# Kernel optimization log

Hardware: AMD Instinct MI355X
Metric: run time of the kernel (lower is better)

Reference implementation:

```python
import jax, jax.numpy as jnp
import numpy as np

B, V, E = 8, 12288, 147456
C_FM, C_U, C_IN, C_HID, C_OUT = 384, 61, 64, 128, 32
EPS = 0.005


def grid_sample_bilinear(img, grid):
    """torch.F.grid_sample, mode='bilinear', padding='zeros', align_corners=False.
    img: (B,C,H,W); grid: (B,Hg,Wg,2) in [-1,1] (x,y). Returns (B,C,Hg,Wg)."""
    Bn, C, H, W = img.shape
    x = (grid[..., 0] + 1.0) * 0.5 * W - 0.5
    y = (grid[..., 1] + 1.0) * 0.5 * H - 0.5
    x0 = jnp.floor(x); y0 = jnp.floor(y)
    wx1 = x - x0; wy1 = y - y0
    wx0 = 1.0 - wx1; wy0 = 1.0 - wy1
    x0i = x0.astype(jnp.int32); y0i = y0.astype(jnp.int32)

    def gather(iy, ix):
        valid = (ix >= 0) & (ix < W) & (iy >= 0) & (iy < H)
        ixc = jnp.clip(ix, 0, W - 1)
        iyc = jnp.clip(iy, 0, H - 1)
        v = jax.vmap(lambda im, yy, xx: im[:, yy, xx])(img, iyc, ixc)  # (B,C,Hg,Wg)
        return v * valid[:, None].astype(img.dtype)

    out = (gather(y0i, x0i) * (wy0 * wx0)[:, None]
           + gather(y0i, x0i + 1) * (wy0 * wx1)[:, None]
           + gather(y0i + 1, x0i) * (wy1 * wx0)[:, None]
           + gather(y0i + 1, x0i + 1) * (wy1 * wx1)[:, None])
    return out


def setup_inputs() -> dict:
    key = jax.random.key(0)
    ks = jax.random.split(key, 12)
    vertices = jax.random.normal(ks[0], (B, V, 3), jnp.float32) * 0.3
    fz = jnp.full((B,), 0.005, jnp.float32) + jax.random.uniform(ks[1], (B,), jnp.float32) * 0.0005
    cz = jax.random.normal(ks[2], (B, 2), jnp.float32) * 0.05
    # depth near fz*(z+100) ~ 0.5 so the |d - z| < eps visibility test fires for a subset
    depth_map = 0.5 + jax.random.normal(ks[3], (B, 1, 128, 128), jnp.float32) * 0.005
    feature_map = jax.random.normal(ks[4], (B, C_FM, 64, 64), jnp.float32)
    conv_w = jax.random.normal(ks[5], (C_U, C_FM), jnp.float32) / np.sqrt(C_FM)
    conv_b = jnp.zeros((C_U,), jnp.float32)
    W1 = jax.random.normal(ks[6], (C_IN, C_HID), jnp.float32) / np.sqrt(C_IN)
    b1 = jnp.zeros((C_HID,), jnp.float32)
    W2 = jax.random.normal(ks[7], (C_HID, C_OUT), jnp.float32) / np.sqrt(C_HID)
    W_dv = jax.random.normal(ks[8], (C_HID, 3), jnp.float32) / np.sqrt(C_HID)
    edge_row = jax.random.randint(ks[9], (E,), 0, V, jnp.int32)
    edge_col = jax.random.randint(ks[10], (E,), 0, V, jnp.int32)
    return {"feature_map": feature_map, "depth_map": depth_map, "vertices": vertices,
            "fz": fz, "cz": cz, "conv_w": conv_w, "conv_b": conv_b,
            "W1": W1, "b1": b1, "W2": W2, "W_dv": W_dv,
            "edge_row": edge_row, "edge_col": edge_col}


def reference(feature_map, depth_map, vertices, fz, cz, conv_w, conv_b,
              W1, b1, W2, W_dv, edge_row, edge_col):
    # ---- indexing(): project vertices to image plane (replicates cz[:,0] on both axes as in source) ----
    v = jnp.stack([vertices[..., 0], vertices[..., 1], vertices[..., 2] + 100.0], axis=-1)
    v = fz[:, None, None] * v
    cshift = cz[:, 0][:, None]
    v = v.at[..., 0].add(cshift).at[..., 1].add(cshift)
    grid = v[:, None, :, :2]                                     # (B,1,V,2)
    sampled_depth = grid_sample_bilinear(depth_map, grid)[:, 0, 0, :]   # (B,V)
    visible = jnp.abs(sampled_depth - v[..., 2]) < EPS           # (B,V) bool
    sf = grid_sample_bilinear(feature_map, grid)[:, :, 0, :]     # (B,C_FM,V)
    sf = sf * visible[:, None, :].astype(sf.dtype)
    # ---- 1x1 conv projection ----
    proj = jnp.einsum('oc,bcv->bov', conv_w, sf) + conv_b[None, :, None]  # (B,C_U,V)
    # ---- GCN input: concat projected features + raw vertex coords ----
    x = jnp.concatenate([proj, jnp.transpose(vertices, (0, 2, 1))], axis=1)  # (B,C_IN,V)
    x = jnp.transpose(x, (0, 2, 1))                              # (B,V,C_IN)
    # ---- sparse-adjacency message passing (row-normalized A) ----
    deg = jax.ops.segment_sum(jnp.ones((E,), x.dtype), edge_row, num_segments=V)
    deg = jnp.maximum(deg, 1.0)

    def agg(h):  # h: (B,V,C) -> A_norm @ h
        msgs = h[:, edge_col]                                    # (B,E,C) gather
        s = jax.vmap(lambda m: jax.ops.segment_sum(m, edge_row, num_segments=V))(msgs)
        return s / deg[None, :, None]

    h = jax.nn.relu(agg(x) @ W1 + b1)                            # (B,V,C_HID)
    x_out = agg(h) @ W2                                          # (B,V,C_OUT)
    dv = h @ W_dv                                                # (B,V,3)
    vertices_new = vertices + dv
    # pack (gcn features, refined verts *1000, offsets *1000) as in source scaling
    return jnp.concatenate([x_out, vertices_new * 1000.0, dv * 1000.0], axis=-1)  # (B,V,38)
```

## Files before the change

kernel.cpp:

```cpp
#include <hip/hip_runtime.h>

#define NB 8
#define NV 12288
#define NE 147456
#define CFM 384
#define CU 61
#define FEPS 0.005f

typedef unsigned short ushort_t;
typedef unsigned int uint_t;
typedef __attribute__((ext_vector_type(8))) unsigned short ushort8v;
typedef __attribute__((ext_vector_type(4))) unsigned short ushort4v;

__device__ inline float b2f(ushort_t u) {
    return __uint_as_float(((uint_t)u) << 16);
}
__device__ inline ushort_t f2b(float f) {
    uint_t u = __float_as_uint(f);
    return (ushort_t)((u + 0x7fffu + ((u >> 16) & 1u)) >> 16);
}

__global__ __launch_bounds__(512) void kL1(const float* __restrict__ cw,
                                           float* __restrict__ cwT,
                                           const int* __restrict__ erow,
                                           int* __restrict__ counts) {
    if (blockIdx.x < 48) {
        int idx = blockIdx.x * 512 + threadIdx.x;
        int c = idx >> 6, o = idx & 63;
        cwT[idx] = (o < CU) ? cw[o * CFM + c] : 0.f;
    } else {
        int e = (blockIdx.x - 48) * 512 + threadIdx.x;
        if (e < NE) atomicAdd(&counts[erow[e]], 1);
    }
}

__device__ void conv_body(int bid, float* smem, const float* __restrict__ fm,
                          const float* __restrict__ cwT, ushort_t* __restrict__ pf) {
    int tid = threadIdx.x;
    int lane = tid & 63;
    int og = __builtin_amdgcn_readfirstlane(tid >> 6);
    int idx0 = bid * 64;
    int b = idx0 >> 12, p0 = idx0 & 4095;
    const float* fb = fm + (size_t)b * CFM * 4096 + p0;
    int sc = tid >> 4, spq = tid & 15;
    const float* saddr = fb + (size_t)sc * 4096 + spq * 4;

    float acc[8];
#pragma unroll
    for (int o = 0; o < 8; o++) acc[o] = 0.f;

    float4 nxt = *(const float4*)saddr;
    int buf = 0;
    for (int cc = 0; cc < CFM; cc += 32) {
        float* ftb = smem + buf * 2048;
        *(float4*)(ftb + sc * 64 + spq * 4) = nxt;
        __syncthreads();
        if (cc + 32 < CFM)
            nxt = *(const float4*)(saddr + (size_t)(cc + 32) * 4096);
#pragma unroll 8
        for (int c = 0; c < 32; c++) {
            float fv = ftb[c * 64 + lane];
            const float4* w4 = (const float4*)(cwT + (cc + c) * 64 + og * 8);
            float4 wa = w4[0], wb = w4[1];
            float w[8] = {wa.x, wa.y, wa.z, wa.w, wb.x, wb.y, wb.z, wb.w};
#pragma unroll
            for (int o = 0; o < 8; o++) acc[o] = fmaf(fv, w[o], acc[o]);
        }
        buf ^= 1;
    }
    uint_t pk[4];
#pragma unroll
    for (int j = 0; j < 4; j++)
        pk[j] = (uint_t)f2b(acc[2 * j]) | ((uint_t)f2b(acc[2 * j + 1]) << 16);
    uint4* outp = (uint4*)(pf + (size_t)(idx0 + lane) * 64 + og * 8);
    outp[0] = make_uint4(pk[0], pk[1], pk[2], pk[3]);
}

__device__ void scan_body(int* ipart, const int* __restrict__ counts,
                          int* __restrict__ offs) {
    int t = threadIdx.x;
    int base = t * 24;
    int local[24];
    int s = 0;
#pragma unroll
    for (int i = 0; i < 24; i++) { local[i] = s; s += counts[base + i]; }
    ipart[t] = s;
    __syncthreads();
    for (int off = 1; off < 512; off <<= 1) {
        int v = (t >= off) ? ipart[t - off] : 0;
        __syncthreads();
        ipart[t] += v;
        __syncthreads();
    }
    int prefix = ipart[t] - s;
#pragma unroll
    for (int i = 0; i < 24; i++) offs[base + i] = prefix + local[i];
}

__global__ __launch_bounds__(512) void kL2(const float* __restrict__ fm,
                                           const float* __restrict__ cwT,
                                           ushort_t* __restrict__ pf,
                                           const int* __restrict__ counts,
                                           int* __restrict__ offs) {
    __shared__ float smem[2 * 32 * 64];
    if (blockIdx.x == 0) {
        scan_body((int*)smem, counts, offs);
    } else {
        conv_body(blockIdx.x - 1, smem, fm, cwT, pf);
    }
}

__device__ void sample_body(int t, const float* __restrict__ depth,
                            const ushort_t* __restrict__ pf,
                            const float* __restrict__ verts,
                            const float* __restrict__ fz,
                            const float* __restrict__ cz,
                            const float* __restrict__ convb,
                            ushort_t* __restrict__ xfeat) {
    int gid = t >> 4;
    int ln = t & 15;
    int b = gid / NV;
    int v = gid - b * NV;
    const float* vp = verts + (size_t)gid * 3;
    float vx = vp[0], vy = vp[1], vz = vp[2];
    float fzb = fz[b], czb = cz[2 * b];
    float gx = fzb * vx + czb;
    float gy = fzb * vy + czb;
    float gz = fzb * (vz + 100.f);

    float px = (gx + 1.f) * 64.f - 0.5f;
    float py = (gy + 1.f) * 64.f - 0.5f;
    float fx0 = floorf(px), fy0 = floorf(py);
    float wx1 = px - fx0, wy1 = py - fy0, wx0 = 1.f - wx1, wy0 = 1.f - wy1;
    int x0 = (int)fx0, y0 = (int)fy0;
    const float* dmb = depth + (size_t)b * 128 * 128;
    float d00 = 0.f, d01 = 0.f, d10 = 0.f, d11 = 0.f;
    bool X0 = (x0 >= 0 && x0 < 128), X1 = (x0 + 1 >= 0 && x0 + 1 < 128);
    bool Y0 = (y0 >= 0 && y0 < 128), Y1 = (y0 + 1 >= 0 && y0 + 1 < 128);
    int xa = min(max(x0, 0), 127), xb = min(max(x0 + 1, 0), 127);
    int ya = min(max(y0, 0), 127), yb = min(max(y0 + 1, 0), 127);
    if (Y0 && X0) d00 = dmb[ya * 128 + xa];
    if (Y0 && X1) d01 = dmb[ya * 128 + xb];
    if (Y1 && X0) d10 = dmb[yb * 128 + xa];
    if (Y1 && X1) d11 = dmb[yb * 128 + xb];
    float sd = d00 * wy0 * wx0 + d01 * wy0 * wx1 + d10 * wy1 * wx0 + d11 * wy1 * wx1;
    float vis = (fabsf(sd - gz) < FEPS) ? 1.f : 0.f;

    float qx = (gx + 1.f) * 32.f - 0.5f;
    float qy = (gy + 1.f) * 32.f - 0.5f;
    float gx0 = floorf(qx), gy0 = floorf(qy);
    float ax1 = qx - gx0, ay1 = qy - gy0, ax0 = 1.f - ax1, ay0 = 1.f - ay1;
    int icx0 = (int)gx0, icy0 = (int)gy0;
    bool FX0 = (icx0 >= 0 && icx0 < 64), FX1 = (icx0 + 1 >= 0 && icx0 + 1 < 64);
    bool FY0 = (icy0 >= 0 && icy0 < 64), FY1 = (icy0 + 1 >= 0 && icy0 + 1 < 64);
    int fxa = min(max(icx0, 0), 63), fxb = min(max(icx0 + 1, 0), 63);
    int fya = min(max(icy0, 0), 63), fyb = min(max(icy0 + 1, 0), 63);
    float m00 = (FY0 && FX0) ? ay0 * ax0 : 0.f;
    float m01 = (FY0 && FX1) ? ay0 * ax1 : 0.f;
    float m10 = (FY1 && FX0) ? ay1 * ax0 : 0.f;
    float m11 = (FY1 && FX1) ? ay1 * ax1 : 0.f;
    const ushort_t* pfb = pf + (size_t)b * 4096 * 64;
    const ushort_t* p00 = pfb + ((size_t)fya * 64 + fxa) * 64;
    const ushort_t* p01 = pfb + ((size_t)fya * 64 + fxb) * 64;
    const ushort_t* p10 = pfb + ((size_t)fyb * 64 + fxa) * 64;
    const ushort_t* p11 = pfb + ((size_t)fyb * 64 + fxb) * 64;

    ushort_t* xr = xfeat + ((size_t)v * NB + b) * 64;
#pragma unroll
    for (int j = 0; j < 4; j++) {
        int c = ln + 16 * j;
        if (c < CU) {
            float val = m00 * b2f(p00[c]) + m01 * b2f(p01[c])
                      + m10 * b2f(p10[c]) + m11 * b2f(p11[c]);
            xr[c] = f2b(vis * val + convb[c]);
        } else {
            xr[c] = f2b(vp[c - CU]);
        }
    }
}

__global__ __launch_bounds__(512) void kL3(const int* __restrict__ erow,
                                           const int* __restrict__ ecol,
                                           const int* __restrict__ offs,
                                           int* __restrict__ cursor,
                                           int* __restrict__ csr,
                                           const float* __restrict__ depth,
                                           const ushort_t* __restrict__ pf,
                                           const float* __restrict__ verts,
                                           const float* __restrict__ fz,
                                           const float* __restrict__ cz,
                                           const float* __restrict__ convb,
                                           ushort_t* __restrict__ xfeat) {
    if (blockIdx.x < 288) {
        int e = blockIdx.x * 512 + threadIdx.x;
        if (e < NE) {
            int r = erow[e];
            int pos = offs[r] + atomicAdd(&cursor[r], 1);
            csr[pos] = ecol[e];
        }
    } else {
        int t = (blockIdx.x - 288) * 512 + threadIdx.x;
        sample_body(t, depth, pf, verts, fz, cz, convb, xfeat);
    }
}

__global__ __launch_bounds__(256) void k_gmlp(
        const int* __restrict__ counts, const int* __restrict__ offs,
        const int* __restrict__ csr, const ushort_t* __restrict__ xfeat,
        const float* __restrict__ W1, const float* __restrict__ b1,
        const float* __restrict__ W2, const float* __restrict__ Wdv,
        const float* __restrict__ verts, ushort_t* __restrict__ y2,
        float* __restrict__ out) {
    __shared__ float smem[2 * 64 * 37];
    float* xl = smem;
    float* part2 = smem;
    int tid = threadIdx.x;
    int lane = tid & 63;
    int w = __builtin_amdgcn_readfirstlane(tid >> 6);
    int vbase = blockIdx.x * 8;

    {
        int vid = vbase + 2 * w;
        int beg0 = offs[vid], n0 = counts[vid];
        int beg1 = offs[vid + 1], n1 = counts[vid + 1];
        float a0[8], a1[8];
#pragma unroll
        for (int t = 0; t < 8; t++) { a0[t] = 0.f; a1[t] = 0.f; }
        int nmax = max(n0, n1);
        for (int j = 0; j < nmax; j++) {
            if (j < n0) {
                int c = csr[beg0 + j];
                ushort8v u = *(const ushort8v*)(xfeat + (size_t)c * 512 + lane * 8);
#pragma unroll
                for (int t = 0; t < 8; t++) a0[t] += b2f(u[t]);
            }
            if (j < n1) {
                int c = csr[beg1 + j];
                ushort8v u = *(const ushort8v*)(xfeat + (size_t)c * 512 + lane * 8);
#pragma unroll
                for (int t = 0; t < 8; t++) a1[t] += b2f(u[t]);
            }
        }
        float d0 = 1.f / fmaxf((float)n0, 1.f);
        float d1 = 1.f / fmaxf((float)n1, 1.f);
        float* dst0 = xl + ((2 * w) * 8 + (lane >> 3)) * 65 + (lane & 7) * 8;
        float* dst1 = xl + ((2 * w + 1) * 8 + (lane >> 3)) * 65 + (lane & 7) * 8;
#pragma unroll
        for (int t = 0; t < 8; t++) dst0[t] = a0[t] * d0;
#pragma unroll
        for (int t = 0; t < 8; t++) dst1[t] = a1[t] * d1;
    }
    __syncthreads();

    float h[32];
    {
        const float* bp = b1 + w * 32;
#pragma unroll
        for (int j = 0; j < 32; j++) h[j] = bp[j];
    }
    const float* xrow = xl + lane * 65;
#pragma unroll 8
    for (int k = 0; k < 64; k++) {
        float xv = xrow[k];
        const float* wk = W1 + k * 128 + w * 32;
#pragma unroll
        for (int j = 0; j < 32; j++) h[j] = fmaf(xv, wk[j], h[j]);
    }
#pragma unroll
    for (int j = 0; j < 32; j++) h[j] = fmaxf(h[j], 0.f);

    float acc2[35];
#pragma unroll
    for (int j = 0; j < 35; j++) acc2[j] = 0.f;
    const float* w2p = W2 + (size_t)(w * 32) * 32;
    const float* wdp = Wdv + (size_t)(w * 32) * 3;
#pragma unroll 4
    for (int kc = 0; kc < 32; kc++) {
        float hv = h[kc];
#pragma unroll
        for (int j = 0; j < 32; j++)
            acc2[j] = fmaf(hv, w2p[kc * 32 + j], acc2[j]);
        acc2[32] = fmaf(hv, wdp[kc * 3 + 0], acc2[32]);
        acc2[33] = fmaf(hv, wdp[kc * 3 + 1], acc2[33]);
        acc2[34] = fmaf(hv, wdp[kc * 3 + 2], acc2[34]);
    }
    __syncthreads();

    if (w >= 2) {
        float* pp = part2 + ((size_t)(w - 2) * 64 + lane) * 37;
#pragma unroll
        for (int j = 0; j < 35; j++) pp[j] = acc2[j];
    }
    __syncthreads();
    if (w < 2) {
        const float* pp = part2 + ((size_t)w * 64 + lane) * 37;
#pragma unroll
        for (int j = 0; j < 35; j++) acc2[j] += pp[j];
    }
    __syncthreads();
    if (w == 1) {
        float* pp = part2 + (size_t)lane * 37;
#pragma unroll
        for (int j = 0; j < 35; j++) pp[j] = acc2[j];
    }
    __syncthreads();
    if (w == 0) {
        const float* pp = part2 + (size_t)lane * 37;
#pragma unroll
        for (int j = 0; j < 35; j++) acc2[j] += pp[j];
        int row = vbase * 8 + lane;
        uint_t pk[16];
#pragma unroll
        for (int j = 0; j < 16; j++)
            pk[j] = (uint_t)f2b(acc2[2 * j]) | ((uint_t)f2b(acc2[2 * j + 1]) << 16);
        uint4* yp = (uint4*)(y2 + (size_t)row * 32);
#pragma unroll
        for (int j = 0; j < 4; j++)
            yp[j] = make_uint4(pk[4 * j], pk[4 * j + 1], pk[4 * j + 2], pk[4 * j + 3]);
        float e0 = acc2[32], e1 = acc2[33], e2 = acc2[34];
        int v = row >> 3, b = row & 7;
        const float* vp = verts + ((size_t)b * NV + v) * 3;
        float* orow = out + ((size_t)b * NV + v) * 38;
        orow[32] = (vp[0] + e0) * 1000.f;
        orow[33] = (vp[1] + e1) * 1000.f;
        orow[34] = (vp[2] + e2) * 1000.f;
        orow[35] = e0 * 1000.f;
        orow[36] = e1 * 1000.f;
        orow[37] = e2 * 1000.f;
    }
}

__global__ void k_agg2(const int* __restrict__ counts, const int* __restrict__ offs,
                       const int* __restrict__ csr, const ushort_t* __restrict__ y2,
                       float* __restrict__ out) {
    int wid = (blockIdx.x * 256 + threadIdx.x) >> 6;
    int l = threadIdx.x & 63;
    if (wid >= NV) return;
    int beg = offs[wid], n = counts[wid];
    float a[4];
#pragma unroll
    for (int t = 0; t < 4; t++) a[t] = 0.f;
    for (int j = 0; j < n; j++) {
        int c = csr[beg + j];
        ushort4v u = *(const ushort4v*)(y2 + (size_t)c * 256 + l * 4);
#pragma unroll
        for (int t = 0; t < 4; t++) a[t] += b2f(u[t]);
    }
    float dinv = 1.f / fmaxf((float)n, 1.f);
    int b = l >> 3, o = (l & 7) * 4;
    float* orow = out + ((size_t)b * NV + wid) * 38 + o;
    orow[0] = a[0] * dinv;
    orow[1] = a[1] * dinv;
    orow[2] = a[2] * dinv;
    orow[3] = a[3] * dinv;
}

extern "C" void kernel_launch(void* const* d_in, const int* in_sizes, int n_in,
                              void* d_out, int out_size, void* d_ws, size_t ws_size,
                              hipStream_t stream) {
    const float* fm  = (const float*)d_in[0];
    const float* dm  = (const float*)d_in[1];
    const float* vt  = (const float*)d_in[2];
    const float* fz  = (const float*)d_in[3];
    const float* cz  = (const float*)d_in[4];
    const float* cw  = (const float*)d_in[5];
    const float* cb  = (const float*)d_in[6];
    const float* W1  = (const float*)d_in[7];
    const float* b1  = (const float*)d_in[8];
    const float* W2  = (const float*)d_in[9];
    const float* Wdv = (const float*)d_in[10];
    const int* erow  = (const int*)d_in[11];
    const int* ecol  = (const int*)d_in[12];
    float* out = (float*)d_out;

    float* ws    = (float*)d_ws;
    float* cwT   = ws;
    ushort_t* pf = (ushort_t*)(cwT + 24576);
    ushort_t* xfeat = (ushort_t*)((float*)pf + 1048576);
    ushort_t* y2 = (ushort_t*)((float*)xfeat + 3145728);
    int* counts  = (int*)((float*)y2 + 1572864);
    int* offs    = counts + 12288;
    int* cursor  = offs + 12288;
    int* csr     = cursor + 12288;

    hipMemsetAsync(counts, 0, 12288 * sizeof(int), stream);
    hipMemsetAsync(cursor, 0, 12288 * sizeof(int), stream);

    kL1<<<336, 512, 0, stream>>>(cw, cwT, erow, counts);
    kL2<<<513, 512, 0, stream>>>(fm, cwT, pf, counts, offs);
    kL3<<<3360, 512, 0, stream>>>(erow, ecol, offs, cursor, csr,
                                  dm, pf, vt, fz, cz, cb, xfeat);
    k_gmlp<<<1536, 256, 0, stream>>>(counts, offs, csr, xfeat,
                                     W1, b1, W2, Wdv, vt, y2, out);
    k_agg2<<<3072, 256, 0, stream>>>(counts, offs, csr, y2, out);
}
```

Before: 143.8 us.

## Split neighbor gathers across wave quarters with 64-byte loads and shuffle reduction

```diff
diff --git a/kernel.cpp b/kernel.cpp
--- a/kernel.cpp
+++ b/kernel.cpp
@@ -10,7 +10,6 @@
 typedef unsigned short ushort_t;
 typedef unsigned int uint_t;
 typedef __attribute__((ext_vector_type(8))) unsigned short ushort8v;
-typedef __attribute__((ext_vector_type(4))) unsigned short ushort4v;
 
 __device__ inline float b2f(ushort_t u) {
     return __uint_as_float(((uint_t)u) << 16);
@@ -219,36 +218,38 @@
     int w = __builtin_amdgcn_readfirstlane(tid >> 6);
     int vbase = blockIdx.x * 8;
 
-    {
-        int vid = vbase + 2 * w;
-        int beg0 = offs[vid], n0 = counts[vid];
-        int beg1 = offs[vid + 1], n1 = counts[vid + 1];
-        float a0[8], a1[8];
-#pragma unroll
-        for (int t = 0; t < 8; t++) { a0[t] = 0.f; a1[t] = 0.f; }
-        int nmax = max(n0, n1);
-        for (int j = 0; j < nmax; j++) {
-            if (j < n0) {
-                int c = csr[beg0 + j];
-                ushort8v u = *(const ushort8v*)(xfeat + (size_t)c * 512 + lane * 8);
-#pragma unroll
-                for (int t = 0; t < 8; t++) a0[t] += b2f(u[t]);
+    int q = lane >> 4, s = lane & 15;
+#pragma unroll
+    for (int vs = 0; vs < 2; vs++) {
+        int vloc = 2 * w + vs;
+        int vid = vbase + vloc;
+        int beg = offs[vid], n = counts[vid];
+        float a[32];
+#pragma unroll
+        for (int t = 0; t < 32; t++) a[t] = 0.f;
+        for (int j = q; j < n; j += 4) {
+            int c = csr[beg + j];
+            const ushort8v* src = (const ushort8v*)(xfeat + (size_t)c * 512 + s * 32);
+            ushort8v u0 = src[0], u1 = src[1], u2 = src[2], u3 = src[3];
+#pragma unroll
+            for (int t = 0; t < 8; t++) {
+                a[t]      += b2f(u0[t]);
+                a[8 + t]  += b2f(u1[t]);
+                a[16 + t] += b2f(u2[t]);
+                a[24 + t] += b2f(u3[t]);
             }
-            if (j < n1) {
-                int c = csr[beg1 + j];
-                ushort8v u = *(const ushort8v*)(xfeat + (size_t)c * 512 + lane * 8);
-#pragma unroll
-                for (int t = 0; t < 8; t++) a1[t] += b2f(u[t]);
-            }
-        }
-        float d0 = 1.f / fmaxf((float)n0, 1.f);
-        float d1 = 1.f / fmaxf((float)n1, 1.f);
-        float* dst0 = xl + ((2 * w) * 8 + (lane >> 3)) * 65 + (lane & 7) * 8;
-        float* dst1 = xl + ((2 * w + 1) * 8 + (lane >> 3)) * 65 + (lane & 7) * 8;
-#pragma unroll
-        for (int t = 0; t < 8; t++) dst0[t] = a0[t] * d0;
-#pragma unroll
-        for (int t = 0; t < 8; t++) dst1[t] = a1[t] * d1;
+        }
+#pragma unroll
+        for (int t = 0; t < 32; t++) {
+            a[t] += __shfl_xor(a[t], 16, 64);
+            a[t] += __shfl_xor(a[t], 32, 64);
+        }
+        if (q == 0) {
+            float dinv = 1.f / fmaxf((float)n, 1.f);
+            float* dst = xl + ((size_t)(vloc * 8 + (s >> 1))) * 65 + (s & 1) * 32;
+#pragma unroll
+            for (int t = 0; t < 32; t++) dst[t] = a[t] * dinv;
+        }
     }
     __syncthreads();
 
@@ -336,23 +337,33 @@
     int wid = (blockIdx.x * 256 + threadIdx.x) >> 6;
     int l = threadIdx.x & 63;
     if (wid >= NV) return;
+    int q = l >> 4, s = l & 15;
     int beg = offs[wid], n = counts[wid];
-    float a[4];
-#pragma unroll
-    for (int t = 0; t < 4; t++) a[t] = 0.f;
-    for (int j = 0; j < n; j++) {
+    float a[16];
+#pragma unroll
+    for (int t = 0; t < 16; t++) a[t] = 0.f;
+    for (int j = q; j < n; j += 4) {
         int c = csr[beg + j];
-        ushort4v u = *(const ushort4v*)(y2 + (size_t)c * 256 + l * 4);
-#pragma unroll
-        for (int t = 0; t < 4; t++) a[t] += b2f(u[t]);
-    }
-    float dinv = 1.f / fmaxf((float)n, 1.f);
-    int b = l >> 3, o = (l & 7) * 4;
-    float* orow = out + ((size_t)b * NV + wid) * 38 + o;
-    orow[0] = a[0] * dinv;
-    orow[1] = a[1] * dinv;
-    orow[2] = a[2] * dinv;
-    orow[3] = a[3] * dinv;
+        const ushort8v* src = (const ushort8v*)(y2 + (size_t)c * 256 + s * 16);
+        ushort8v u0 = src[0], u1 = src[1];
+#pragma unroll
+        for (int t = 0; t < 8; t++) {
+            a[t]     += b2f(u0[t]);
+            a[8 + t] += b2f(u1[t]);
+        }
+    }
+#pragma unroll
+    for (int t = 0; t < 16; t++) {
+        a[t] += __shfl_xor(a[t], 16, 64);
+        a[t] += __shfl_xor(a[t], 32, 64);
+    }
+    if (q == 0) {
+        float dinv = 1.f / fmaxf((float)n, 1.f);
+        int b = s >> 1, ch0 = (s & 1) * 16;
+        float* orow = out + ((size_t)b * NV + wid) * 38 + ch0;
+#pragma unroll
+        for (int t = 0; t < 16; t++) orow[t] = a[t] * dinv;
+    }
 }
 
 extern "C" void kernel_launch(void* const* d_in, const int* in_sizes, int n_in,
```

Result: no change. 143.8 us (+0.1%).
